# Kernel optimization log

Measured on AMD Instinct MI355X. Metric: run time of the kernel, lower is better.

## Reference

```python
import jax, jax.numpy as jnp
import numpy as np

N = 20000
E = 500000
IN, HID, OUT = 128, 128, 64
NEG_SLOPE = 0.01  # torch F.leaky_relu default


def setup_inputs() -> dict:
    key = jax.random.key(0)
    ks = jax.random.split(key, 16)
    d = {}
    d['x'] = jax.random.normal(ks[0], (N, IN), dtype=jnp.float32)
    # layer1 per-etype params (torch Linear convention: W is (out,in))
    d['W1_0'] = jax.random.normal(ks[1], (HID, IN), dtype=jnp.float32) / np.sqrt(IN)
    d['b1_0'] = jnp.zeros((HID,), jnp.float32)
    d['a1_0'] = jax.random.normal(ks[2], (2 * HID,), dtype=jnp.float32) / np.sqrt(2 * HID)
    d['W1_1'] = jax.random.normal(ks[3], (HID, IN), dtype=jnp.float32) / np.sqrt(IN)
    d['b1_1'] = jnp.zeros((HID,), jnp.float32)
    d['a1_1'] = jax.random.normal(ks[4], (2 * HID,), dtype=jnp.float32) / np.sqrt(2 * HID)
    # layer2 per-etype params
    d['W2_0'] = jax.random.normal(ks[5], (OUT, HID), dtype=jnp.float32) / np.sqrt(HID)
    d['b2_0'] = jnp.zeros((OUT,), jnp.float32)
    d['a2_0'] = jax.random.normal(ks[6], (2 * OUT,), dtype=jnp.float32) / np.sqrt(2 * OUT)
    d['W2_1'] = jax.random.normal(ks[7], (OUT, HID), dtype=jnp.float32) / np.sqrt(HID)
    d['b2_1'] = jnp.zeros((OUT,), jnp.float32)
    d['a2_1'] = jax.random.normal(ks[8], (2 * OUT,), dtype=jnp.float32) / np.sqrt(2 * OUT)
    # edge lists per etype
    d['src0'] = jax.random.randint(ks[9], (E,), 0, N, dtype=jnp.int32)
    d['dst0'] = jax.random.randint(ks[10], (E,), 0, N, dtype=jnp.int32)
    d['src1'] = jax.random.randint(ks[11], (E,), 0, N, dtype=jnp.int32)
    d['dst1'] = jax.random.randint(ks[12], (E,), 0, N, dtype=jnp.int32)
    return d


def _att_layer(x, Ws, bs, avs, srcs, dsts, n_nodes):
    """One AttHeteroRGCNLayer: per-etype linear + GAT attention + segment
    softmax over destination + weighted sum, then cross-etype sum."""
    h = jnp.zeros((n_nodes, Ws[0].shape[0]), x.dtype)
    for W, b, a, src, dst in zip(Ws, bs, avs, srcs, dsts):
        Wh = x @ W.T + b                       # [N, out]
        out = Wh.shape[1]
        # attn_fc(concat[Wh_src, Wh_dst]) = Wh_src@a_l + Wh_dst@a_r
        al = Wh @ a[:out]                      # [N]
        ar = Wh @ a[out:]                      # [N]
        e = jax.nn.leaky_relu(al[src] + ar[dst], NEG_SLOPE)  # [E]
        # segment softmax over incoming edges of each destination node
        m = jax.ops.segment_max(e, dst, num_segments=n_nodes)  # [N]
        ex = jnp.exp(e - m[dst])
        denom = jax.ops.segment_sum(ex, dst, num_segments=n_nodes)  # [N]
        alpha = ex / denom[dst]                # [E]
        # attention-weighted sum of gathered src messages
        h = h + jax.ops.segment_sum(alpha[:, None] * Wh[src], dst,
                                    num_segments=n_nodes)
    return h


def reference(x, W1_0, b1_0, a1_0, W1_1, b1_1, a1_1,
              W2_0, b2_0, a2_0, W2_1, b2_1, a2_1,
              src0, dst0, src1, dst1):
    srcs = [src0, src1]
    dsts = [dst0, dst1]
    h1 = _att_layer(x, [W1_0, W1_1], [b1_0, b1_1], [a1_0, a1_1], srcs, dsts, N)
    h1 = jax.nn.leaky_relu(h1, NEG_SLOPE)
    h2 = _att_layer(h1, [W2_0, W2_1], [b2_0, b2_1], [a2_0, a2_1], srcs, dsts, N)
    return h2
```

## Files before the change

### kernel.cpp

```cpp
#include <hip/hip_runtime.h>
#include <hip/hip_bf16.h>

#define NNODES 20000
#define NEDGES 500000
#define LRELU(v) ((v) > 0.f ? (v) : (v) * 0.01f)

using bf16_t = __hip_bfloat16;
typedef unsigned short u16;
typedef __attribute__((ext_vector_type(8))) short bf16x8;
typedef __attribute__((ext_vector_type(4))) float f32x4;

__device__ inline float bf2f(short u) {
  unsigned int i = ((unsigned int)(unsigned short)u) << 16;
  float f;
  __builtin_memcpy(&f, &i, 4);
  return f;
}

constexpr int HB = (NEDGES + 255) / 256;
constexpr int SBX = (NNODES * 128 / 4 + 255) / 256;
constexpr int SBW1 = (128 * 128 / 4 + 255) / 256;
constexpr int SBW2 = (64 * 128 / 4 + 255) / 256;
constexpr int GB = (NNODES + 63) / 64;

__device__ inline void histpos_body(int bb, int t, const int* dst0,
                                    const int* dst1, int* deg, u16* pos0,
                                    u16* pos1) {
  const int* dst = t ? dst1 : dst0;
  u16* pos = t ? pos1 : pos0;
  int* d = deg + t * NNODES;
  int i = bb * 256 + threadIdx.x;
  if (i < NEDGES) pos[i] = (u16)atomicAdd(&d[dst[i]], 1);
}

__device__ inline void split_body(const float* in, bf16_t* hi, bf16_t* lo,
                                  int i, int n4) {
  if (i >= n4) return;
  float4 v = *(const float4*)&in[i * 4];
  bf16_t h0 = __float2bfloat16(v.x), h1 = __float2bfloat16(v.y);
  bf16_t h2 = __float2bfloat16(v.z), h3 = __float2bfloat16(v.w);
  hi[i * 4 + 0] = h0;
  hi[i * 4 + 1] = h1;
  hi[i * 4 + 2] = h2;
  hi[i * 4 + 3] = h3;
  lo[i * 4 + 0] = __float2bfloat16(v.x - __bfloat162float(h0));
  lo[i * 4 + 1] = __float2bfloat16(v.y - __bfloat162float(h1));
  lo[i * 4 + 2] = __float2bfloat16(v.z - __bfloat162float(h2));
  lo[i * 4 + 3] = __float2bfloat16(v.w - __bfloat162float(h3));
}

__device__ inline void scatter_body(int bb, int t, const int* src0,
                                    const int* dst0, const int* src1,
                                    const int* dst1, const u16* pos0,
                                    const u16* pos1, const int* row_off,
                                    u16* srt0, u16* srt1) {
  const int* src = t ? src1 : src0;
  const int* dst = t ? dst1 : dst0;
  const u16* pos = t ? pos1 : pos0;
  const int* ro = row_off + t * (NNODES + 1);
  u16* srt = t ? srt1 : srt0;
  int i = bb * 256 + threadIdx.x;
  if (i < NEDGES) {
    int dd = dst[i];
    srt[ro[dd] + (int)pos[i]] = (u16)src[i];
  }
}

template <int F>
__device__ inline void gemm_body(
    int bx, int t, const bf16_t* Xh, const bf16_t* Xl, const bf16_t* Wh0,
    const bf16_t* Wl0, const bf16_t* Wh1, const bf16_t* Wl1, const float* b0p,
    const float* b1p, const float* a0p, const float* a1p, bf16_t* Y0,
    bf16_t* Y1, float* al0, float* ar0, float* al1, float* ar1, int nrows) {
  constexpr int NT = F / 16;
  const bf16_t* Wgh = t ? Wh1 : Wh0;
  const bf16_t* Wgl = t ? Wl1 : Wl0;
  const float* bias = t ? b1p : b0p;
  const float* av = t ? a1p : a0p;
  bf16_t* Y = t ? Y1 : Y0;
  float* al = t ? al1 : al0;
  float* ar = t ? ar1 : ar0;

  int wid = threadIdx.x >> 6, lane = threadIdx.x & 63;
  int row0 = bx * 64 + wid * 16;
  int cl = lane & 15, g4 = lane >> 4;
  int rAc = min(row0 + cl, nrows - 1);

  f32x4 acc[NT] = {};

#pragma unroll
  for (int ks = 0; ks < 4; ++ks) {
    int k0 = ks * 32 + g4 * 8;
    bf16x8 Ah = *(const bf16x8*)&Xh[(size_t)rAc * 128 + k0];
    bf16x8 Al = *(const bf16x8*)&Xl[(size_t)rAc * 128 + k0];
#pragma unroll
    for (int nt = 0; nt < NT; ++nt) {
      size_t off = (size_t)(nt * 16 + cl) * 128 + k0;
      bf16x8 Bh = *(const bf16x8*)&Wgh[off];
      bf16x8 Bl = *(const bf16x8*)&Wgl[off];
      acc[nt] = __builtin_amdgcn_mfma_f32_16x16x32_bf16(Ah, Bh, acc[nt], 0, 0, 0);
      acc[nt] = __builtin_amdgcn_mfma_f32_16x16x32_bf16(Ah, Bl, acc[nt], 0, 0, 0);
      acc[nt] = __builtin_amdgcn_mfma_f32_16x16x32_bf16(Al, Bh, acc[nt], 0, 0, 0);
    }
  }

  float pl[4] = {}, pr[4] = {};
#pragma unroll
  for (int nt = 0; nt < NT; ++nt) {
    int c = nt * 16 + cl;
    float bv = bias[c], aL = av[c], aR = av[F + c];
#pragma unroll
    for (int j = 0; j < 4; ++j) {
      int r = row0 + g4 * 4 + j;
      float v = acc[nt][j] + bv;
      if (r < nrows) Y[(size_t)r * F + c] = __float2bfloat16(v);
      pl[j] += v * aL;
      pr[j] += v * aR;
    }
  }
#pragma unroll
  for (int j = 0; j < 4; ++j) {
    float sl = pl[j], sr = pr[j];
#pragma unroll
    for (int o = 8; o; o >>= 1) {
      sl += __shfl_xor(sl, o);
      sr += __shfl_xor(sr, o);
    }
    int r = row0 + g4 * 4 + j;
    if (cl == 0 && r < nrows) {
      al[r] = sl;
      ar[r] = sr;
    }
  }
}

__global__ __launch_bounds__(256) void k_pre(
    const int* __restrict__ dst0, const int* __restrict__ dst1,
    int* __restrict__ deg, u16* __restrict__ pos0, u16* __restrict__ pos1,
    const float* __restrict__ x, bf16_t* __restrict__ xh,
    bf16_t* __restrict__ xl, const float* __restrict__ W1_0,
    bf16_t* __restrict__ w1h0, bf16_t* __restrict__ w1l0,
    const float* __restrict__ W1_1, bf16_t* __restrict__ w1h1,
    bf16_t* __restrict__ w1l1, const float* __restrict__ W2_0,
    bf16_t* __restrict__ w2h0, bf16_t* __restrict__ w2l0,
    const float* __restrict__ W2_1, bf16_t* __restrict__ w2h1,
    bf16_t* __restrict__ w2l1) {
  int b = blockIdx.x;
  if (b < 2 * HB) {
    histpos_body(b >= HB ? b - HB : b, b >= HB, dst0, dst1, deg, pos0, pos1);
    return;
  }
  b -= 2 * HB;
  int tid = threadIdx.x;
  if (b < SBX) { split_body(x, xh, xl, b * 256 + tid, NNODES * 128 / 4); return; }
  b -= SBX;
  if (b < SBW1) { split_body(W1_0, w1h0, w1l0, b * 256 + tid, 128 * 128 / 4); return; }
  b -= SBW1;
  if (b < SBW1) { split_body(W1_1, w1h1, w1l1, b * 256 + tid, 128 * 128 / 4); return; }
  b -= SBW1;
  if (b < SBW2) { split_body(W2_0, w2h0, w2l0, b * 256 + tid, 64 * 128 / 4); return; }
  b -= SBW2;
  split_body(W2_1, w2h1, w2l1, b * 256 + tid, 64 * 128 / 4);
}

__global__ __launch_bounds__(1024) void k_scan(const int* __restrict__ deg,
                                               int* __restrict__ row_off,
                                               int n) {
  deg += blockIdx.x * n;
  row_off += blockIdx.x * (n + 1);
  constexpr int PT = 20;
  __shared__ int wsum[16];
  int tid = threadIdx.x, wid = tid >> 6, lane = tid & 63;
  int base_i = tid * PT;
  int v[PT];
  int s = 0;
#pragma unroll
  for (int q = 0; q < PT; ++q) {
    int i = base_i + q;
    v[q] = (i < n) ? deg[i] : 0;
    s += v[q];
  }
  int x = s;
#pragma unroll
  for (int o = 1; o < 64; o <<= 1) {
    int t = __shfl_up(x, o);
    if (lane >= o) x += t;
  }
  if (lane == 63) wsum[wid] = x;
  __syncthreads();
  if (wid == 0) {
    int ws = (lane < 16) ? wsum[lane] : 0;
#pragma unroll
    for (int o = 1; o < 16; o <<= 1) {
      int t = __shfl_up(ws, o);
      if (lane >= o) ws += t;
    }
    if (lane < 16) wsum[lane] = ws;
  }
  __syncthreads();
  int run = (wid ? wsum[wid - 1] : 0) + (x - s);
#pragma unroll
  for (int q = 0; q < PT; ++q) {
    int i = base_i + q;
    if (i < n) row_off[i] = run;
    run += v[q];
  }
  if (tid == 1023) row_off[n] = run;
}

__global__ __launch_bounds__(256) void k_mid(
    const bf16_t* __restrict__ xh, const bf16_t* __restrict__ xl,
    const bf16_t* __restrict__ w1h0, const bf16_t* __restrict__ w1l0,
    const bf16_t* __restrict__ w1h1, const bf16_t* __restrict__ w1l1,
    const float* __restrict__ b1_0, const float* __restrict__ b1_1,
    const float* __restrict__ a1_0, const float* __restrict__ a1_1,
    bf16_t* __restrict__ Whb_0, bf16_t* __restrict__ Whb_1,
    float* __restrict__ alA, float* __restrict__ arA, float* __restrict__ alB,
    float* __restrict__ arB, const int* __restrict__ src0,
    const int* __restrict__ dst0, const int* __restrict__ src1,
    const int* __restrict__ dst1, const u16* __restrict__ pos0,
    const u16* __restrict__ pos1, const int* __restrict__ row_off,
    u16* __restrict__ srt0, u16* __restrict__ srt1) {
  int b = blockIdx.x;
  if (b < 2 * GB) {
    gemm_body<128>(b >= GB ? b - GB : b, b >= GB, xh, xl, w1h0, w1l0, w1h1,
                   w1l1, b1_0, b1_1, a1_0, a1_1, Whb_0, Whb_1, alA, arA, alB,
                   arB, NNODES);
    return;
  }
  b -= 2 * GB;
  scatter_body(b >= HB ? b - HB : b, b >= HB, src0, dst0, src1, dst1, pos0,
               pos1, row_off, srt0, srt1);
}

__global__ __launch_bounds__(256) void k_gemm64(
    const bf16_t* __restrict__ Xh, const bf16_t* __restrict__ Xl,
    const bf16_t* __restrict__ w2h0, const bf16_t* __restrict__ w2l0,
    const bf16_t* __restrict__ w2h1, const bf16_t* __restrict__ w2l1,
    const float* __restrict__ b2_0, const float* __restrict__ b2_1,
    const float* __restrict__ a2_0, const float* __restrict__ a2_1,
    bf16_t* __restrict__ Y0, bf16_t* __restrict__ Y1, float* __restrict__ al0,
    float* __restrict__ ar0, float* __restrict__ al1,
    float* __restrict__ ar1) {
  gemm_body<64>(blockIdx.x, blockIdx.y, Xh, Xl, w2h0, w2l0, w2h1, w2l1, b2_0,
                b2_1, a2_0, a2_1, Y0, Y1, al0, ar0, al1, ar1, NNODES);
}

template <int F, int OMODE>
__global__ __launch_bounds__(256) void k_agg2(
    const int* __restrict__ row_off, const u16* __restrict__ srt0,
    const u16* __restrict__ srt1, const float* __restrict__ al0,
    const float* __restrict__ ar0, const float* __restrict__ al1,
    const float* __restrict__ ar1, const bf16_t* __restrict__ Wg0,
    const bf16_t* __restrict__ Wg1, float* __restrict__ H,
    bf16_t* __restrict__ Hh, bf16_t* __restrict__ Hl, int n) {
  constexpr int LPR = (F * 2) / 16;
  constexpr int NGR = 64 / LPR;
  constexpr int VE = F / LPR;
  int wid = threadIdx.x >> 6, lane = threadIdx.x & 63;
  int d = blockIdx.x * 4 + wid;
  if (d >= n) return;
  int g = lane / LPR, cl = lane % LPR;
  float acc[VE] = {};

#pragma unroll
  for (int t = 0; t < 2; ++t) {
    const int* ro = row_off + t * (n + 1);
    const u16* srt = t ? srt1 : srt0;
    const float* al = t ? al1 : al0;
    const float* ar = t ? ar1 : ar0;
    const bf16_t* Wg = t ? Wg1 : Wg0;
    int beg = ro[d], end = ro[d + 1];
    if (beg == end) continue;
    float ard = ar[d];

    float denT = 0.f;
    float accT[VE] = {};
    int j = beg + g;
    for (; j + NGR < end; j += 2 * NGR) {
      int s0 = srt[j], s1 = srt[j + NGR];
      float e0 = fminf(LRELU(al[s0] + ard), 70.f);
      float e1 = fminf(LRELU(al[s1] + ard), 70.f);
      float w0 = __expf(e0), w1 = __expf(e1);
      denT += w0 + w1;
      bf16x8 r0 = *(const bf16x8*)&Wg[(size_t)s0 * F + cl * 8];
      bf16x8 r1 = *(const bf16x8*)&Wg[(size_t)s1 * F + cl * 8];
#pragma unroll
      for (int v = 0; v < VE; ++v)
        accT[v] += w0 * bf2f(r0[v]) + w1 * bf2f(r1[v]);
    }
    if (j < end) {
      int s0 = srt[j];
      float e0 = fminf(LRELU(al[s0] + ard), 70.f);
      float w0 = __expf(e0);
      denT += w0;
      bf16x8 r0 = *(const bf16x8*)&Wg[(size_t)s0 * F + cl * 8];
#pragma unroll
      for (int v = 0; v < VE; ++v) accT[v] += w0 * bf2f(r0[v]);
    }

#pragma unroll
    for (int o = 32; o >= LPR; o >>= 1) {
      denT += __shfl_xor(denT, o);
#pragma unroll
      for (int v = 0; v < VE; ++v) accT[v] += __shfl_xor(accT[v], o);
    }
    float rden = 1.f / denT;
#pragma unroll
    for (int v = 0; v < VE; ++v) acc[v] += accT[v] * rden;
  }

  if (g == 0) {
    if (OMODE == 0) {
#pragma unroll
      for (int q = 0; q < VE; q += 4) {
        float4 o4 = make_float4(acc[q], acc[q + 1], acc[q + 2], acc[q + 3]);
        *(float4*)&H[(size_t)d * F + cl * VE + q] = o4;
      }
    } else {
      bf16x8 hv, lv;
#pragma unroll
      for (int q = 0; q < VE; ++q) {
        float v = LRELU(acc[q]);
        bf16_t h = __float2bfloat16(v);
        bf16_t l = __float2bfloat16(v - __bfloat162float(h));
        short hb, lb;
        __builtin_memcpy(&hb, &h, 2);
        __builtin_memcpy(&lb, &l, 2);
        hv[q] = hb;
        lv[q] = lb;
      }
      *(bf16x8*)&Hh[(size_t)d * F + cl * 8] = hv;
      *(bf16x8*)&Hl[(size_t)d * F + cl * 8] = lv;
    }
  }
}

extern "C" void kernel_launch(void* const* d_in, const int* in_sizes, int n_in,
                              void* d_out, int out_size, void* d_ws,
                              size_t ws_size, hipStream_t stream) {
  const float* x    = (const float*)d_in[0];
  const float* W1_0 = (const float*)d_in[1];
  const float* b1_0 = (const float*)d_in[2];
  const float* a1_0 = (const float*)d_in[3];
  const float* W1_1 = (const float*)d_in[4];
  const float* b1_1 = (const float*)d_in[5];
  const float* a1_1 = (const float*)d_in[6];
  const float* W2_0 = (const float*)d_in[7];
  const float* b2_0 = (const float*)d_in[8];
  const float* a2_0 = (const float*)d_in[9];
  const float* W2_1 = (const float*)d_in[10];
  const float* b2_1 = (const float*)d_in[11];
  const float* a2_1 = (const float*)d_in[12];
  const int* src0 = (const int*)d_in[13];
  const int* dst0 = (const int*)d_in[14];
  const int* src1 = (const int*)d_in[15];
  const int* dst1 = (const int*)d_in[16];
  float* out = (float*)d_out;

  const int N = NNODES, E = NEDGES;

  char* w = (char*)d_ws;
  auto alloc = [&](size_t bytes) -> char* {
    char* p = w;
    w += (bytes + 255) & ~(size_t)255;
    return p;
  };
  int* row_off = (int*)alloc(2 * (N + 1) * sizeof(int));
  int* deg     = (int*)alloc(2 * N * sizeof(int));
  u16* pos0    = (u16*)alloc((size_t)E * 2);
  u16* pos1    = (u16*)alloc((size_t)E * 2);
  u16* srt0    = (u16*)alloc((size_t)E * 2);
  u16* srt1    = (u16*)alloc((size_t)E * 2);
  bf16_t* xh   = (bf16_t*)alloc((size_t)N * 128 * 2);
  bf16_t* xl   = (bf16_t*)alloc((size_t)N * 128 * 2);
  bf16_t* Whb_0 = (bf16_t*)alloc((size_t)N * 128 * 2);
  bf16_t* Whb_1 = (bf16_t*)alloc((size_t)N * 128 * 2);
  bf16_t* h1h  = (bf16_t*)alloc((size_t)N * 128 * 2);
  bf16_t* h1l  = (bf16_t*)alloc((size_t)N * 128 * 2);
  bf16_t* w1h0 = (bf16_t*)alloc(128 * 128 * 2);
  bf16_t* w1l0 = (bf16_t*)alloc(128 * 128 * 2);
  bf16_t* w1h1 = (bf16_t*)alloc(128 * 128 * 2);
  bf16_t* w1l1 = (bf16_t*)alloc(128 * 128 * 2);
  bf16_t* w2h0 = (bf16_t*)alloc(64 * 128 * 2);
  bf16_t* w2l0 = (bf16_t*)alloc(64 * 128 * 2);
  bf16_t* w2h1 = (bf16_t*)alloc(64 * 128 * 2);
  bf16_t* w2l1 = (bf16_t*)alloc(64 * 128 * 2);
  bf16_t* Wh2b_0 = (bf16_t*)alloc((size_t)N * 64 * 2);
  bf16_t* Wh2b_1 = (bf16_t*)alloc((size_t)N * 64 * 2);
  float* alA   = (float*)alloc(N * sizeof(float));
  float* arA   = (float*)alloc(N * sizeof(float));
  float* alB   = (float*)alloc(N * sizeof(float));
  float* arB   = (float*)alloc(N * sizeof(float));
  (void)ws_size;

  hipMemsetAsync(deg, 0, 2 * N * sizeof(int), stream);

  int preg = 2 * HB + SBX + 2 * SBW1 + 2 * SBW2;
  k_pre<<<preg, 256, 0, stream>>>(dst0, dst1, deg, pos0, pos1, x, xh, xl,
                                  W1_0, w1h0, w1l0, W1_1, w1h1, w1l1, W2_0,
                                  w2h0, w2l0, W2_1, w2h1, w2l1);
  k_scan<<<2, 1024, 0, stream>>>(deg, row_off, N);
  int midg = 2 * GB + 2 * HB;
  k_mid<<<midg, 256, 0, stream>>>(xh, xl, w1h0, w1l0, w1h1, w1l1, b1_0, b1_1,
                                  a1_0, a1_1, Whb_0, Whb_1, alA, arA, alB,
                                  arB, src0, dst0, src1, dst1, pos0, pos1,
                                  row_off, srt0, srt1);
  int ngrid4 = (N + 3) / 4;
  k_agg2<128, 1><<<ngrid4, 256, 0, stream>>>(
      row_off, srt0, srt1, alA, arA, alB, arB, Whb_0, Whb_1, nullptr, h1h,
      h1l, N);
  k_gemm64<<<dim3(GB, 2), 256, 0, stream>>>(h1h, h1l, w2h0, w2l0, w2h1, w2l1,
                                            b2_0, b2_1, a2_0, a2_1, Wh2b_0,
                                            Wh2b_1, alA, arA, alB, arB);
  k_agg2<64, 0><<<ngrid4, 256, 0, stream>>>(
      row_off, srt0, srt1, alA, arA, alB, arB, Wh2b_0, Wh2b_1, out, nullptr,
      nullptr, N);
}
```

Before: 257.3 us.

## Privatize degree histogram into 8 replicas to reduce atomic contention

```diff
diff --git a/kernel.cpp b/kernel.cpp
--- a/kernel.cpp
+++ b/kernel.cpp
@@ -8,6 +8,7 @@
 using bf16_t = __hip_bfloat16;
 typedef unsigned short u16;
 typedef __attribute__((ext_vector_type(8))) short bf16x8;
+typedef __attribute__((ext_vector_type(8))) unsigned short u16x8;
 typedef __attribute__((ext_vector_type(4))) float f32x4;
 
 __device__ inline float bf2f(short u) {
@@ -23,14 +24,15 @@
 constexpr int SBW2 = (64 * 128 / 4 + 255) / 256;
 constexpr int GB = (NNODES + 63) / 64;
 
-__device__ inline void histpos_body(int bb, int t, const int* dst0,
-                                    const int* dst1, int* deg, u16* pos0,
+__device__ inline void histpos_body(int bb, int t, int grp, const int* dst0,
+                                    const int* dst1, int* deg8, u16* pos0,
                                     u16* pos1) {
   const int* dst = t ? dst1 : dst0;
   u16* pos = t ? pos1 : pos0;
-  int* d = deg + t * NNODES;
+  int* d = deg8 + (grp * 2 + t) * NNODES;
   int i = bb * 256 + threadIdx.x;
-  if (i < NEDGES) pos[i] = (u16)atomicAdd(&d[dst[i]], 1);
+  if (i < NEDGES)
+    pos[i] = (u16)((grp << 13) | atomicAdd(&d[dst[i]], 1));
 }
 
 __device__ inline void split_body(const float* in, bf16_t* hi, bf16_t* lo,
@@ -53,7 +55,7 @@
                                     const int* dst0, const int* src1,
                                     const int* dst1, const u16* pos0,
                                     const u16* pos1, const int* row_off,
-                                    u16* srt0, u16* srt1) {
+                                    const u16* base8, u16* srt0, u16* srt1) {
   const int* src = t ? src1 : src0;
   const int* dst = t ? dst1 : dst0;
   const u16* pos = t ? pos1 : pos0;
@@ -62,7 +64,10 @@
   int i = bb * 256 + threadIdx.x;
   if (i < NEDGES) {
     int dd = dst[i];
-    srt[ro[dd] + (int)pos[i]] = (u16)src[i];
+    u16 p = pos[i];
+    int grp = p >> 13, rank = p & 8191;
+    int base = (int)base8[(size_t)(t * NNODES + dd) * 8 + grp];
+    srt[ro[dd] + base + rank] = (u16)src[i];
   }
 }
 
@@ -136,7 +141,7 @@
 
 __global__ __launch_bounds__(256) void k_pre(
     const int* __restrict__ dst0, const int* __restrict__ dst1,
-    int* __restrict__ deg, u16* __restrict__ pos0, u16* __restrict__ pos1,
+    int* __restrict__ deg8, u16* __restrict__ pos0, u16* __restrict__ pos1,
     const float* __restrict__ x, bf16_t* __restrict__ xh,
     bf16_t* __restrict__ xl, const float* __restrict__ W1_0,
     bf16_t* __restrict__ w1h0, bf16_t* __restrict__ w1l0,
@@ -145,9 +150,11 @@
     bf16_t* __restrict__ w2h0, bf16_t* __restrict__ w2l0,
     const float* __restrict__ W2_1, bf16_t* __restrict__ w2h1,
     bf16_t* __restrict__ w2l1) {
+  int grp = blockIdx.x & 7;
   int b = blockIdx.x;
   if (b < 2 * HB) {
-    histpos_body(b >= HB ? b - HB : b, b >= HB, dst0, dst1, deg, pos0, pos1);
+    histpos_body(b >= HB ? b - HB : b, b >= HB, grp, dst0, dst1, deg8, pos0,
+                 pos1);
     return;
   }
   b -= 2 * HB;
@@ -163,11 +170,12 @@
   split_body(W2_1, w2h1, w2l1, b * 256 + tid, 64 * 128 / 4);
 }
 
-__global__ __launch_bounds__(1024) void k_scan(const int* __restrict__ deg,
+__global__ __launch_bounds__(1024) void k_scan(const int* __restrict__ deg8,
                                                int* __restrict__ row_off,
+                                               u16* __restrict__ base8,
                                                int n) {
-  deg += blockIdx.x * n;
-  row_off += blockIdx.x * (n + 1);
+  int t = blockIdx.x;
+  row_off += t * (n + 1);
   constexpr int PT = 20;
   __shared__ int wsum[16];
   int tid = threadIdx.x, wid = tid >> 6, lane = tid & 63;
@@ -177,14 +185,24 @@
 #pragma unroll
   for (int q = 0; q < PT; ++q) {
     int i = base_i + q;
-    v[q] = (i < n) ? deg[i] : 0;
-    s += v[q];
+    int tot = 0;
+    if (i < n) {
+      u16x8 bv;
+#pragma unroll
+      for (int g = 0; g < 8; ++g) {
+        bv[g] = (u16)tot;
+        tot += deg8[(g * 2 + t) * n + i];
+      }
+      *(u16x8*)&base8[(size_t)(t * n + i) * 8] = bv;
+    }
+    v[q] = tot;
+    s += tot;
   }
   int x = s;
 #pragma unroll
   for (int o = 1; o < 64; o <<= 1) {
-    int t = __shfl_up(x, o);
-    if (lane >= o) x += t;
+    int tt = __shfl_up(x, o);
+    if (lane >= o) x += tt;
   }
   if (lane == 63) wsum[wid] = x;
   __syncthreads();
@@ -192,8 +210,8 @@
     int ws = (lane < 16) ? wsum[lane] : 0;
 #pragma unroll
     for (int o = 1; o < 16; o <<= 1) {
-      int t = __shfl_up(ws, o);
-      if (lane >= o) ws += t;
+      int tt = __shfl_up(ws, o);
+      if (lane >= o) ws += tt;
     }
     if (lane < 16) wsum[lane] = ws;
   }
@@ -220,7 +238,8 @@
     const int* __restrict__ dst0, const int* __restrict__ src1,
     const int* __restrict__ dst1, const u16* __restrict__ pos0,
     const u16* __restrict__ pos1, const int* __restrict__ row_off,
-    u16* __restrict__ srt0, u16* __restrict__ srt1) {
+    const u16* __restrict__ base8, u16* __restrict__ srt0,
+    u16* __restrict__ srt1) {
   int b = blockIdx.x;
   if (b < 2 * GB) {
     gemm_body<128>(b >= GB ? b - GB : b, b >= GB, xh, xl, w1h0, w1l0, w1h1,
@@ -230,7 +249,7 @@
   }
   b -= 2 * GB;
   scatter_body(b >= HB ? b - HB : b, b >= HB, src0, dst0, src1, dst1, pos0,
-               pos1, row_off, srt0, srt1);
+               pos1, row_off, base8, srt0, srt1);
 }
 
 __global__ __launch_bounds__(256) void k_gemm64(
@@ -367,7 +386,8 @@
     return p;
   };
   int* row_off = (int*)alloc(2 * (N + 1) * sizeof(int));
-  int* deg     = (int*)alloc(2 * N * sizeof(int));
+  int* deg8    = (int*)alloc(8 * 2 * N * sizeof(int));
+  u16* base8   = (u16*)alloc((size_t)2 * N * 8 * 2);
   u16* pos0    = (u16*)alloc((size_t)E * 2);
   u16* pos1    = (u16*)alloc((size_t)E * 2);
   u16* srt0    = (u16*)alloc((size_t)E * 2);
@@ -394,18 +414,18 @@
   float* arB   = (float*)alloc(N * sizeof(float));
   (void)ws_size;
 
-  hipMemsetAsync(deg, 0, 2 * N * sizeof(int), stream);
+  hipMemsetAsync(deg8, 0, 8 * 2 * N * sizeof(int), stream);
 
   int preg = 2 * HB + SBX + 2 * SBW1 + 2 * SBW2;
-  k_pre<<<preg, 256, 0, stream>>>(dst0, dst1, deg, pos0, pos1, x, xh, xl,
+  k_pre<<<preg, 256, 0, stream>>>(dst0, dst1, deg8, pos0, pos1, x, xh, xl,
                                   W1_0, w1h0, w1l0, W1_1, w1h1, w1l1, W2_0,
                                   w2h0, w2l0, W2_1, w2h1, w2l1);
-  k_scan<<<2, 1024, 0, stream>>>(deg, row_off, N);
+  k_scan<<<2, 1024, 0, stream>>>(deg8, row_off, base8, N);
   int midg = 2 * GB + 2 * HB;
   k_mid<<<midg, 256, 0, stream>>>(xh, xl, w1h0, w1l0, w1h1, w1l1, b1_0, b1_1,
                                   a1_0, a1_1, Whb_0, Whb_1, alA, arA, alB,
                                   arB, src0, dst0, src1, dst1, pos0, pos1,
-                                  row_off, srt0, srt1);
+                                  row_off, base8, srt0, srt1);
   int ngrid4 = (N + 3) / 4;
   k_agg2<128, 1><<<ngrid4, 256, 0, stream>>>(
       row_off, srt0, srt1, alA, arA, alB, arB, Whb_0, Whb_1, nullptr, h1h,
```

Result: slower. 320.7 us (+24.6%).

## Build degree histogram in LDS with packed counters and fuse scan with split

Applied to the files above, without the earlier changes.

```diff
diff --git a/kernel.cpp b/kernel.cpp
--- a/kernel.cpp
+++ b/kernel.cpp
@@ -7,30 +7,63 @@
 
 using bf16_t = __hip_bfloat16;
 typedef unsigned short u16;
+typedef unsigned int u32;
 typedef __attribute__((ext_vector_type(8))) short bf16x8;
 typedef __attribute__((ext_vector_type(4))) float f32x4;
 
 __device__ inline float bf2f(short u) {
-  unsigned int i = ((unsigned int)(unsigned short)u) << 16;
+  u32 i = ((u32)(u16)u) << 16;
   float f;
   __builtin_memcpy(&f, &i, 4);
   return f;
 }
 
+constexpr int CHUNK = NEDGES / 4;
 constexpr int HB = (NEDGES + 255) / 256;
-constexpr int SBX = (NNODES * 128 / 4 + 255) / 256;
-constexpr int SBW1 = (128 * 128 / 4 + 255) / 256;
-constexpr int SBW2 = (64 * 128 / 4 + 255) / 256;
 constexpr int GB = (NNODES + 63) / 64;
-
-__device__ inline void histpos_body(int bb, int t, const int* dst0,
-                                    const int* dst1, int* deg, u16* pos0,
-                                    u16* pos1) {
+constexpr int SBX = NNODES * 128 / 4 / 1024;
+constexpr int SBW1 = 128 * 128 / 4 / 1024;
+constexpr int SBW2 = 64 * 128 / 4 / 1024;
+
+__global__ __launch_bounds__(1024) void k_ldshist(const int* __restrict__ dst0,
+                                                  const int* __restrict__ dst1,
+                                                  int* __restrict__ deg,
+                                                  u16* __restrict__ pos0,
+                                                  u16* __restrict__ pos1) {
+  __shared__ u32 hist[NNODES / 2];
+  int b = blockIdx.x;
+  int t = b >> 2, chunk = b & 3;
   const int* dst = t ? dst1 : dst0;
   u16* pos = t ? pos1 : pos0;
-  int* d = deg + t * NNODES;
-  int i = bb * 256 + threadIdx.x;
-  if (i < NEDGES) pos[i] = (u16)atomicAdd(&d[dst[i]], 1);
+  int* dg = deg + t * NNODES;
+  int tid = threadIdx.x;
+
+  for (int i = tid; i < NNODES / 2; i += 1024) hist[i] = 0;
+  __syncthreads();
+
+  int beg = chunk * CHUNK, end = beg + CHUNK;
+  for (int i = beg + tid; i < end; i += 1024) {
+    int d = dst[i];
+    int sh = (d & 1) * 16;
+    u32 old = atomicAdd(&hist[d >> 1], 1u << sh);
+    pos[i] = (u16)((old >> sh) & 0xFFFFu);
+  }
+  __syncthreads();
+
+  for (int i = tid; i < NNODES / 2; i += 1024) {
+    u32 wv = hist[i];
+    u32 c0 = wv & 0xFFFFu, c1 = wv >> 16;
+    u32 b0 = c0 ? (u32)atomicAdd(&dg[2 * i], (int)c0) : 0u;
+    u32 b1 = c1 ? (u32)atomicAdd(&dg[2 * i + 1], (int)c1) : 0u;
+    hist[i] = b0 | (b1 << 16);
+  }
+  __syncthreads();
+
+  for (int i = beg + tid; i < end; i += 1024) {
+    int d = dst[i];
+    int sh = (d & 1) * 16;
+    pos[i] = (u16)(pos[i] + ((hist[d >> 1] >> sh) & 0xFFFFu));
+  }
 }
 
 __device__ inline void split_body(const float* in, bf16_t* hi, bf16_t* lo,
@@ -49,6 +82,73 @@
   lo[i * 4 + 3] = __float2bfloat16(v.w - __bfloat162float(h3));
 }
 
+__global__ __launch_bounds__(1024) void k_scansplit(
+    const int* __restrict__ deg, int* __restrict__ row_off,
+    const float* __restrict__ x, bf16_t* __restrict__ xh,
+    bf16_t* __restrict__ xl, const float* __restrict__ W1_0,
+    bf16_t* __restrict__ w1h0, bf16_t* __restrict__ w1l0,
+    const float* __restrict__ W1_1, bf16_t* __restrict__ w1h1,
+    bf16_t* __restrict__ w1l1, const float* __restrict__ W2_0,
+    bf16_t* __restrict__ w2h0, bf16_t* __restrict__ w2l0,
+    const float* __restrict__ W2_1, bf16_t* __restrict__ w2h1,
+    bf16_t* __restrict__ w2l1) {
+  int b = blockIdx.x;
+  int tid = threadIdx.x;
+  if (b < 2) {
+    const int* tot = deg + b * NNODES;
+    int* ro = row_off + b * (NNODES + 1);
+    constexpr int PT = 20;
+    __shared__ int wsum[16];
+    int wid = tid >> 6, lane = tid & 63;
+    int base_i = tid * PT;
+    int v[PT];
+    int s = 0;
+#pragma unroll
+    for (int q = 0; q < PT; ++q) {
+      int i = base_i + q;
+      v[q] = (i < NNODES) ? tot[i] : 0;
+      s += v[q];
+    }
+    int xx = s;
+#pragma unroll
+    for (int o = 1; o < 64; o <<= 1) {
+      int tv = __shfl_up(xx, o);
+      if (lane >= o) xx += tv;
+    }
+    if (lane == 63) wsum[wid] = xx;
+    __syncthreads();
+    if (wid == 0) {
+      int ws = (lane < 16) ? wsum[lane] : 0;
+#pragma unroll
+      for (int o = 1; o < 16; o <<= 1) {
+        int tv = __shfl_up(ws, o);
+        if (lane >= o) ws += tv;
+      }
+      if (lane < 16) wsum[lane] = ws;
+    }
+    __syncthreads();
+    int run = (wid ? wsum[wid - 1] : 0) + (xx - s);
+#pragma unroll
+    for (int q = 0; q < PT; ++q) {
+      int i = base_i + q;
+      if (i < NNODES) ro[i] = run;
+      run += v[q];
+    }
+    if (tid == 1023) ro[NNODES] = run;
+    return;
+  }
+  b -= 2;
+  if (b < SBX) { split_body(x, xh, xl, b * 1024 + tid, NNODES * 128 / 4); return; }
+  b -= SBX;
+  if (b < SBW1) { split_body(W1_0, w1h0, w1l0, b * 1024 + tid, 128 * 128 / 4); return; }
+  b -= SBW1;
+  if (b < SBW1) { split_body(W1_1, w1h1, w1l1, b * 1024 + tid, 128 * 128 / 4); return; }
+  b -= SBW1;
+  if (b < SBW2) { split_body(W2_0, w2h0, w2l0, b * 1024 + tid, 64 * 128 / 4); return; }
+  b -= SBW2;
+  split_body(W2_1, w2h1, w2l1, b * 1024 + tid, 64 * 128 / 4);
+}
+
 __device__ inline void scatter_body(int bb, int t, const int* src0,
                                     const int* dst0, const int* src1,
                                     const int* dst1, const u16* pos0,
@@ -132,80 +232,6 @@
       ar[r] = sr;
     }
   }
-}
-
-__global__ __launch_bounds__(256) void k_pre(
-    const int* __restrict__ dst0, const int* __restrict__ dst1,
-    int* __restrict__ deg, u16* __restrict__ pos0, u16* __restrict__ pos1,
-    const float* __restrict__ x, bf16_t* __restrict__ xh,
-    bf16_t* __restrict__ xl, const float* __restrict__ W1_0,
-    bf16_t* __restrict__ w1h0, bf16_t* __restrict__ w1l0,
-    const float* __restrict__ W1_1, bf16_t* __restrict__ w1h1,
-    bf16_t* __restrict__ w1l1, const float* __restrict__ W2_0,
-    bf16_t* __restrict__ w2h0, bf16_t* __restrict__ w2l0,
-    const float* __restrict__ W2_1, bf16_t* __restrict__ w2h1,
-    bf16_t* __restrict__ w2l1) {
-  int b = blockIdx.x;
-  if (b < 2 * HB) {
-    histpos_body(b >= HB ? b - HB : b, b >= HB, dst0, dst1, deg, pos0, pos1);
-    return;
-  }
-  b -= 2 * HB;
-  int tid = threadIdx.x;
-  if (b < SBX) { split_body(x, xh, xl, b * 256 + tid, NNODES * 128 / 4); return; }
-  b -= SBX;
-  if (b < SBW1) { split_body(W1_0, w1h0, w1l0, b * 256 + tid, 128 * 128 / 4); return; }
-  b -= SBW1;
-  if (b < SBW1) { split_body(W1_1, w1h1, w1l1, b * 256 + tid, 128 * 128 / 4); return; }
-  b -= SBW1;
-  if (b < SBW2) { split_body(W2_0, w2h0, w2l0, b * 256 + tid, 64 * 128 / 4); return; }
-  b -= SBW2;
-  split_body(W2_1, w2h1, w2l1, b * 256 + tid, 64 * 128 / 4);
-}
-
-__global__ __launch_bounds__(1024) void k_scan(const int* __restrict__ deg,
-                                               int* __restrict__ row_off,
-                                               int n) {
-  deg += blockIdx.x * n;
-  row_off += blockIdx.x * (n + 1);
-  constexpr int PT = 20;
-  __shared__ int wsum[16];
-  int tid = threadIdx.x, wid = tid >> 6, lane = tid & 63;
-  int base_i = tid * PT;
-  int v[PT];
-  int s = 0;
-#pragma unroll
-  for (int q = 0; q < PT; ++q) {
-    int i = base_i + q;
-    v[q] = (i < n) ? deg[i] : 0;
-    s += v[q];
-  }
-  int x = s;
-#pragma unroll
-  for (int o = 1; o < 64; o <<= 1) {
-    int t = __shfl_up(x, o);
-    if (lane >= o) x += t;
-  }
-  if (lane == 63) wsum[wid] = x;
-  __syncthreads();
-  if (wid == 0) {
-    int ws = (lane < 16) ? wsum[lane] : 0;
-#pragma unroll
-    for (int o = 1; o < 16; o <<= 1) {
-      int t = __shfl_up(ws, o);
-      if (lane >= o) ws += t;
-    }
-    if (lane < 16) wsum[lane] = ws;
-  }
-  __syncthreads();
-  int run = (wid ? wsum[wid - 1] : 0) + (x - s);
-#pragma unroll
-  for (int q = 0; q < PT; ++q) {
-    int i = base_i + q;
-    if (i < n) row_off[i] = run;
-    run += v[q];
-  }
-  if (tid == 1023) row_off[n] = run;
 }
 
 __global__ __launch_bounds__(256) void k_mid(
@@ -396,11 +422,11 @@
 
   hipMemsetAsync(deg, 0, 2 * N * sizeof(int), stream);
 
-  int preg = 2 * HB + SBX + 2 * SBW1 + 2 * SBW2;
-  k_pre<<<preg, 256, 0, stream>>>(dst0, dst1, deg, pos0, pos1, x, xh, xl,
-                                  W1_0, w1h0, w1l0, W1_1, w1h1, w1l1, W2_0,
-                                  w2h0, w2l0, W2_1, w2h1, w2l1);
-  k_scan<<<2, 1024, 0, stream>>>(deg, row_off, N);
+  k_ldshist<<<8, 1024, 0, stream>>>(dst0, dst1, deg, pos0, pos1);
+  int ssg = 2 + SBX + 2 * SBW1 + 2 * SBW2;
+  k_scansplit<<<ssg, 1024, 0, stream>>>(deg, row_off, x, xh, xl, W1_0, w1h0,
+                                        w1l0, W1_1, w1h1, w1l1, W2_0, w2h0,
+                                        w2l0, W2_1, w2h1, w2l1);
   int midg = 2 * GB + 2 * HB;
   k_mid<<<midg, 256, 0, stream>>>(xh, xl, w1h0, w1l0, w1h1, w1l1, b1_0, b1_1,
                                   a1_0, a1_1, Whb_0, Whb_1, alA, arA, alB,
```

Measured after the change: 281.5 us. +9.4%, slower.
